# Kernel optimization log

Measured on AMD Instinct MI355X. Metric: run time of the kernel, lower is better.

## Reference

```python
import jax, jax.numpy as jnp
import numpy as np

B = 32768          # batch
LATENT = 128       # latent_dim
H = 100            # hidden_size
VOCAB = 20         # VOCAB_SIZE_EXPRESSION
EXPR_LEN = 21      # EXPR_LENGTH_EXPRESSION


def setup_inputs() -> dict:
    key = jax.random.key(0)
    ks = jax.random.split(key, 17)
    s = 0.1
    inp = {
        "encoder_hidden": jax.random.normal(ks[0], (B, LATENT), jnp.float32),
        "w_proj": s * jax.random.normal(ks[1], (H, LATENT), jnp.float32),
        "b_proj": s * jax.random.normal(ks[2], (H,), jnp.float32),
        "wih0": s * jax.random.normal(ks[3], (3 * H, H), jnp.float32),
        "whh0": s * jax.random.normal(ks[4], (3 * H, H), jnp.float32),
        "bih0": s * jax.random.normal(ks[5], (3 * H,), jnp.float32),
        "bhh0": s * jax.random.normal(ks[6], (3 * H,), jnp.float32),
        "wih1": s * jax.random.normal(ks[7], (3 * H, H), jnp.float32),
        "whh1": s * jax.random.normal(ks[8], (3 * H, H), jnp.float32),
        "bih1": s * jax.random.normal(ks[9], (3 * H,), jnp.float32),
        "bhh1": s * jax.random.normal(ks[10], (3 * H,), jnp.float32),
        "wih2": s * jax.random.normal(ks[11], (3 * H, H), jnp.float32),
        "whh2": s * jax.random.normal(ks[12], (3 * H, H), jnp.float32),
        "bih2": s * jax.random.normal(ks[13], (3 * H,), jnp.float32),
        "bhh2": s * jax.random.normal(ks[14], (3 * H,), jnp.float32),
        "w_out": s * jax.random.normal(ks[15], (VOCAB, H), jnp.float32),
        "b_out": s * jax.random.normal(ks[16], (VOCAB,), jnp.float32),
    }
    return inp


def _gru_cell(gx, h, whh, bhh):
    # gx: precomputed input gates [B, 3H]; h: [B, H]
    gh = h @ whh.T + bhh
    gxr, gxz, gxn = jnp.split(gx, 3, axis=-1)
    ghr, ghz, ghn = jnp.split(gh, 3, axis=-1)
    r = jax.nn.sigmoid(gxr + ghr)
    z = jax.nn.sigmoid(gxz + ghz)
    n = jnp.tanh(gxn + r * ghn)
    return (1.0 - z) * n + z * h


def reference(encoder_hidden, w_proj, b_proj,
              wih0, whh0, bih0, bhh0,
              wih1, whh1, bih1, bhh1,
              wih2, whh2, bih2, bhh2,
              w_out, b_out):
    # decoder_context: same input fed to the GRU at every timestep
    x0 = encoder_hidden @ w_proj.T + b_proj            # [B, H]
    gx0 = x0 @ wih0.T + bih0                           # layer-0 input gates, constant over time

    h_init = jnp.zeros((3, x0.shape[0], H), x0.dtype)  # (num_layers, B, H)

    def step(carry, _):
        h0, h1, h2 = carry
        h0n = _gru_cell(gx0, h0, whh0, bhh0)
        gx1 = h0n @ wih1.T + bih1
        h1n = _gru_cell(gx1, h1, whh1, bhh1)
        gx2 = h1n @ wih2.T + bih2
        h2n = _gru_cell(gx2, h2, whh2, bhh2)
        logits = h2n @ w_out.T + b_out                 # [B, VOCAB]
        return (h0n, h1n, h2n), logits

    _, outs = jax.lax.scan(step, (h_init[0], h_init[1], h_init[2]), None, length=EXPR_LEN)
    return jnp.transpose(outs, (1, 0, 2))              # [B, EXPR_LEN, VOCAB]
```

## Files before the change

kernel.cpp:

```cpp
#include <hip/hip_runtime.h>


#define NTHR 512
#define NBLK 256
#define ROWS_PB 128

#define OFF_PROJ 0
#define OFF_IH0  14336
#define OFF_HH0  57344
#define OFF_IH1  100352
#define OFF_HH1  143360
#define OFF_IH2  186368
#define OFF_HH2  229376
#define OFF_OUT  272384
#define WP_TOTAL 276480

#define X0_OFF   0
#define H0_OFF   16384
#define H1_OFF   32768
#define H2_OFF   49152
#define SMEM_U16 65536

using frag8 = __attribute__((ext_vector_type(8))) short;
using frag4 = __attribute__((ext_vector_type(4))) short;
using f32x4 = __attribute__((ext_vector_type(4))) float;

struct G4 { frag8 a, b, c, d; };

__device__ __forceinline__ unsigned short f2b(float f) {
    union { float f; unsigned u; } v; v.f = f;
    unsigned r = v.u + 0x7FFF + ((v.u >> 16) & 1);
    return (unsigned short)(r >> 16);
}
__device__ __forceinline__ float b2f(unsigned short b) {
    union { unsigned u; float f; } v; v.u = ((unsigned)b) << 16; return v.f;
}

__device__ __forceinline__ f32x4 mfma32(frag8 a, frag8 b, f32x4 c) {
    return __builtin_amdgcn_mfma_f32_16x16x32_bf16(a, b, c, 0, 0, 0);
}
__device__ __forceinline__ f32x4 dot4(const G4& w, const G4& s, f32x4 acc) {
    acc = mfma32(w.a, s.a, acc); acc = mfma32(w.b, s.b, acc);
    acc = mfma32(w.c, s.c, acc); return mfma32(w.d, s.d, acc);
}
__device__ __forceinline__ void pin(G4& w) {
    asm volatile("" : "+v"(w.a), "+v"(w.b), "+v"(w.c), "+v"(w.d));
}

__global__ void prep_kernel(const float* __restrict__ w_proj,
    const float* __restrict__ wih0, const float* __restrict__ bih0,
    const float* __restrict__ whh0, const float* __restrict__ bhh0,
    const float* __restrict__ wih1, const float* __restrict__ bih1,
    const float* __restrict__ whh1, const float* __restrict__ bhh1,
    const float* __restrict__ wih2, const float* __restrict__ bih2,
    const float* __restrict__ whh2, const float* __restrict__ bhh2,
    const float* __restrict__ w_out, const float* __restrict__ b_out,
    unsigned short* __restrict__ dst)
{
    const float LOG2E  = 1.4426950408889634f;
    const float LOG2E2 = 2.8853900817779268f;
    int idx = blockIdx.x * 256 + threadIdx.x;
    if (idx >= WP_TOTAL) return;
    float v = 0.f;
    if (idx < OFF_IH0) {
        int n = idx >> 7, k = idx & 127;
        if (n < 100) v = w_proj[n * 128 + k];
    } else if (idx < OFF_OUT) {
        int r = idx - OFF_IH0;
        int mi = r / 43008;
        int e  = r - mi * 43008;
        int n = e >> 7, k = e & 127;
        int g = n / 112, nn = n - g * 112;
        if (nn < 100) {
            const float* W; const float* Bv;
            switch (mi) {
                case 0: W = wih0; Bv = bih0; break;
                case 1: W = whh0; Bv = bhh0; break;
                case 2: W = wih1; Bv = bih1; break;
                case 3: W = whh1; Bv = bhh1; break;
                case 4: W = wih2; Bv = bih2; break;
                default: W = whh2; Bv = bhh2; break;
            }
            if (k < 100) v = W[(g * 100 + nn) * 100 + k];
            else if (k == 100) v = Bv[g * 100 + nn];
            v *= (g == 2) ? LOG2E2 : LOG2E;
        }
    } else {
        int e = idx - OFF_OUT;
        int n = e >> 7, k = e & 127;
        if (n < 20) {
            if (k < 100) v = w_out[n * 100 + k];
            else if (k == 100) v = b_out[n];
        }
    }
    dst[idx] = f2b(v);
}

__device__ __forceinline__ int hsw(int buf, int grp, int r, int cu) {
    int row = grp * 16 + r;
    return buf + row * 128 + ((((cu >> 3) ^ (row & 7)) << 3) | (cu & 7));
}
__device__ __forceinline__ G4 ldSG4(const unsigned short* sm, int buf, int grp, int c16, int g4) {
    const unsigned short* p = sm + buf + (grp * 16 + c16) * 128;
    int x = c16 & 7;
    G4 s;
    s.a = *(const frag8*)(p + ((g4 ^ x) << 3));
    s.b = *(const frag8*)(p + (((4 + g4) ^ x) << 3));
    s.c = *(const frag8*)(p + (((8 + g4) ^ x) << 3));
    s.d = *(const frag8*)(p + (((12 + g4) ^ x) << 3));
    return s;
}

__device__ __forceinline__ G4 ldWG4(const unsigned short* __restrict__ m, int g, int ro, int g4) {
    const unsigned short* p = m + (size_t)(g * 112 + ro) * 128 + g4 * 8;
    G4 w;
    w.a = *(const frag8*)p;        w.b = *(const frag8*)(p + 32);
    w.c = *(const frag8*)(p + 64); w.d = *(const frag8*)(p + 96);
    return w;
}

__device__ __forceinline__ void logits_one(const unsigned short* sm,
        const G4& O0, const G4& O1, int grp, int lt,
        float* __restrict__ out, int rbase, int c16, int g4) {
    G4 L = ldSG4(sm, H2_OFF, grp, c16, g4);
    f32x4 a0 = {0.f, 0.f, 0.f, 0.f}, a1 = a0;
    a0 = dot4(O0, L, a0);
    a1 = dot4(O1, L, a1);
    float* po = out + (size_t)(rbase + grp * 16 + c16) * 420 + lt * 20;
    *(f32x4*)(po + g4 * 4) = a0;
    if (g4 == 0) *(f32x4*)(po + 16) = a1;
}

template<bool PH0>
__device__ __forceinline__ void gru_phase(unsigned short* sm, int HS, int HD,
    const unsigned short* __restrict__ wih, const unsigned short* __restrict__ whh,
    const G4* O, int lt, float* __restrict__ out, int rbase,
    bool owner, bool vald, int c16, int g4, int ro, int nbase)
{
    __syncthreads();
    frag4 rp[8], zp[8], hn[8];
    if (owner) {
        G4 Wi = ldWG4(wih, 0, ro, g4), Wh = ldWG4(whh, 0, ro, g4);
        pin(Wi); pin(Wh);
#pragma unroll
        for (int grp = 0; grp < 8; ++grp) {
            G4 S = ldSG4(sm, HS, grp, c16, g4);
            G4 D = ldSG4(sm, HD, grp, c16, g4);
            f32x4 a = {0.f, 0.f, 0.f, 0.f};
            a = dot4(Wi, S, a); a = dot4(Wh, D, a);
#pragma unroll
            for (int j = 0; j < 4; ++j)
                rp[grp][j] = (short)f2b(__builtin_amdgcn_rcpf(1.f + __builtin_amdgcn_exp2f(-a[j])));
        }
        Wi = ldWG4(wih, 1, ro, g4); Wh = ldWG4(whh, 1, ro, g4);
        pin(Wi); pin(Wh);
#pragma unroll
        for (int grp = 0; grp < 8; ++grp) {
            G4 S = ldSG4(sm, HS, grp, c16, g4);
            G4 D = ldSG4(sm, HD, grp, c16, g4);
            f32x4 a = {0.f, 0.f, 0.f, 0.f};
            a = dot4(Wi, S, a); a = dot4(Wh, D, a);
#pragma unroll
            for (int j = 0; j < 4; ++j)
                zp[grp][j] = (short)f2b(__builtin_amdgcn_rcpf(1.f + __builtin_amdgcn_exp2f(-a[j])));
        }
        Wi = ldWG4(wih, 2, ro, g4); Wh = ldWG4(whh, 2, ro, g4);
        pin(Wi); pin(Wh);
#pragma unroll
        for (int grp = 0; grp < 8; ++grp) {
            G4 S = ldSG4(sm, HS, grp, c16, g4);
            G4 D = ldSG4(sm, HD, grp, c16, g4);
            f32x4 ax = {0.f, 0.f, 0.f, 0.f}, ah = ax;
            ax = dot4(Wi, S, ax); ah = dot4(Wh, D, ah);
            frag4 hold = *(const frag4*)(sm + hsw(HD, grp, c16, nbase));
#pragma unroll
            for (int j = 0; j < 4; ++j) {
                float r  = b2f((unsigned short)rp[grp][j]);
                float z  = b2f((unsigned short)zp[grp][j]);
                float y  = ax[j] + r * ah[j];
                float nn = 1.f - 2.f * __builtin_amdgcn_rcpf(1.f + __builtin_amdgcn_exp2f(y));
                float ho = b2f((unsigned short)hold[j]);
                hn[grp][j] = (short)f2b(nn + z * (ho - nn));
            }
        }
    } else if (PH0 && lt >= 0) {
#pragma unroll 1
        for (int grp = 0; grp < 8; ++grp)
            logits_one(sm, O[0], O[1], grp, lt, out, rbase, c16, g4);
    }
    __syncthreads();
    if (owner && vald) {
#pragma unroll
        for (int grp = 0; grp < 8; ++grp)
            *(frag4*)(sm + hsw(HD, grp, c16, nbase)) = hn[grp];
    }
}

__global__ void __launch_bounds__(NTHR, 2) rnn_kernel(
    const float* __restrict__ enc,
    const float* __restrict__ b_proj,
    const unsigned short* __restrict__ wp,
    float* __restrict__ out)
{
    __shared__ unsigned short sm[SMEM_U16];
    const int tid  = threadIdx.x;
    const int lane = tid & 63;
    const int wid  = tid >> 6;
    const int c16  = lane & 15;
    const int g4   = lane >> 4;
    const int rbase = blockIdx.x * ROWS_PB;
    const bool owner = (wid < 7);
    const int tw    = owner ? wid : 0;
    const int ro    = tw * 16 + c16;
    const int nbase = tw * 16 + g4 * 4;
    const bool vald = owner && (nbase < 100);

    for (int i = tid; i < SMEM_U16; i += NTHR) {
        int r  = (i >> 7) & 127;
        int cu = i & 127;
        int lcol = ((((cu >> 3) ^ (r & 7)) << 3) | (cu & 7));
        sm[i] = (lcol == 100) ? (unsigned short)0x3F80 : (unsigned short)0;
    }

    G4 O[2];
    if (!owner) {
        O[0] = ldWG4(wp + OFF_OUT, 0, c16, g4);
        O[1] = ldWG4(wp + OFF_OUT, 0, 16 + c16, g4);
        pin(O[0]); pin(O[1]);
    }
    __syncthreads();

    if (owner) {
        G4 P = ldWG4(wp + OFF_PROJ, 0, ro, g4);
        f32x4 bp = {0.f, 0.f, 0.f, 0.f};
        if (vald) bp = *(const f32x4*)(b_proj + nbase);
#pragma unroll 1
        for (int grp = 0; grp < 8; ++grp) {
            const float* ep = enc + (size_t)(rbase + grp * 16 + c16) * 128 + g4 * 8;
            G4 E;
            {
                frag8 e0, e1, e2, e3;
#pragma unroll
                for (int j = 0; j < 8; ++j) {
                    e0[j] = (short)f2b(ep[j]);      e1[j] = (short)f2b(ep[32 + j]);
                    e2[j] = (short)f2b(ep[64 + j]); e3[j] = (short)f2b(ep[96 + j]);
                }
                E.a = e0; E.b = e1; E.c = e2; E.d = e3;
            }
            f32x4 acc = dot4(P, E, bp);
            if (vald) {
                frag4 xv;
#pragma unroll
                for (int j = 0; j < 4; ++j) xv[j] = (short)f2b(acc[j]);
                *(frag4*)(sm + hsw(X0_OFF, grp, c16, nbase)) = xv;
            }
        }
    }

#pragma unroll 1
    for (int t = 0; t < 21; ++t) {
        gru_phase<true >(sm, X0_OFF, H0_OFF, wp + OFF_IH0, wp + OFF_HH0,
                         O, t - 1, out, rbase, owner, vald, c16, g4, ro, nbase);
        gru_phase<false>(sm, H0_OFF, H1_OFF, wp + OFF_IH1, wp + OFF_HH1,
                         O, -1, out, rbase, owner, vald, c16, g4, ro, nbase);
        gru_phase<false>(sm, H1_OFF, H2_OFF, wp + OFF_IH2, wp + OFF_HH2,
                         O, -1, out, rbase, owner, vald, c16, g4, ro, nbase);
    }

    __syncthreads();
    if (!owner) {
#pragma unroll 1
        for (int grp = 0; grp < 8; ++grp)
            logits_one(sm, O[0], O[1], grp, 20, out, rbase, c16, g4);
    }
}

extern "C" void kernel_launch(void* const* d_in, const int* in_sizes, int n_in,
                              void* d_out, int out_size, void* d_ws, size_t ws_size,
                              hipStream_t stream) {
    const float* enc    = (const float*)d_in[0];
    const float* w_proj = (const float*)d_in[1];
    const float* b_proj = (const float*)d_in[2];
    const float* wih0   = (const float*)d_in[3];
    const float* whh0   = (const float*)d_in[4];
    const float* bih0   = (const float*)d_in[5];
    const float* bhh0   = (const float*)d_in[6];
    const float* wih1   = (const float*)d_in[7];
    const float* whh1   = (const float*)d_in[8];
    const float* bih1   = (const float*)d_in[9];
    const float* bhh1   = (const float*)d_in[10];
    const float* wih2   = (const float*)d_in[11];
    const float* whh2   = (const float*)d_in[12];
    const float* bih2   = (const float*)d_in[13];
    const float* bhh2   = (const float*)d_in[14];
    const float* w_out  = (const float*)d_in[15];
    const float* b_out  = (const float*)d_in[16];
    unsigned short* wpd = (unsigned short*)d_ws;
    float* out          = (float*)d_out;

    prep_kernel<<<(WP_TOTAL + 255) / 256, 256, 0, stream>>>(
        w_proj, wih0, bih0, whh0, bhh0, wih1, bih1, whh1, bhh1,
        wih2, bih2, whh2, bhh2, w_out, b_out, wpd);

    rnn_kernel<<<NBLK, NTHR, 0, stream>>>(enc, b_proj, wpd, out);
}
```

Measured before the change: 524.7 us.

## Double block size and split row groups across two wave sets

Raises the block to 1024 threads with 16 waves, so two sets of 8 waves each handle half of the 128 rows (4 row groups instead of 8). Each set has 7 GRU-owner waves and its own logits wave. This halves the per-wave serial work and register arrays per phase, but moves from 2 blocks per CU to 1 block per CU. The aim is shorter critical paths between barriers, at the cost of loading the weights twice per block and syncing more waves at each barrier.

```diff
diff --git a/kernel.cpp b/kernel.cpp
--- a/kernel.cpp
+++ b/kernel.cpp
@@ -1,9 +1,10 @@
 #include <hip/hip_runtime.h>
 
 
-#define NTHR 512
+#define NTHR 1024
 #define NBLK 256
 #define ROWS_PB 128
+#define NGRP 4
 
 #define OFF_PROJ 0
 #define OFF_IH0  14336
@@ -135,39 +136,42 @@
 __device__ __forceinline__ void gru_phase(unsigned short* sm, int HS, int HD,
     const unsigned short* __restrict__ wih, const unsigned short* __restrict__ whh,
     const G4* O, int lt, float* __restrict__ out, int rbase,
-    bool owner, bool vald, int c16, int g4, int ro, int nbase)
+    bool owner, bool vald, bool logw, int gbase, int c16, int g4, int ro, int nbase)
 {
     __syncthreads();
-    frag4 rp[8], zp[8], hn[8];
+    frag4 rp[NGRP], zp[NGRP], hn[NGRP];
     if (owner) {
         G4 Wi = ldWG4(wih, 0, ro, g4), Wh = ldWG4(whh, 0, ro, g4);
         pin(Wi); pin(Wh);
 #pragma unroll
-        for (int grp = 0; grp < 8; ++grp) {
+        for (int q = 0; q < NGRP; ++q) {
+            int grp = gbase + q;
             G4 S = ldSG4(sm, HS, grp, c16, g4);
             G4 D = ldSG4(sm, HD, grp, c16, g4);
             f32x4 a = {0.f, 0.f, 0.f, 0.f};
             a = dot4(Wi, S, a); a = dot4(Wh, D, a);
 #pragma unroll
             for (int j = 0; j < 4; ++j)
-                rp[grp][j] = (short)f2b(__builtin_amdgcn_rcpf(1.f + __builtin_amdgcn_exp2f(-a[j])));
+                rp[q][j] = (short)f2b(__builtin_amdgcn_rcpf(1.f + __builtin_amdgcn_exp2f(-a[j])));
         }
         Wi = ldWG4(wih, 1, ro, g4); Wh = ldWG4(whh, 1, ro, g4);
         pin(Wi); pin(Wh);
 #pragma unroll
-        for (int grp = 0; grp < 8; ++grp) {
+        for (int q = 0; q < NGRP; ++q) {
+            int grp = gbase + q;
             G4 S = ldSG4(sm, HS, grp, c16, g4);
             G4 D = ldSG4(sm, HD, grp, c16, g4);
             f32x4 a = {0.f, 0.f, 0.f, 0.f};
             a = dot4(Wi, S, a); a = dot4(Wh, D, a);
 #pragma unroll
             for (int j = 0; j < 4; ++j)
-                zp[grp][j] = (short)f2b(__builtin_amdgcn_rcpf(1.f + __builtin_amdgcn_exp2f(-a[j])));
+                zp[q][j] = (short)f2b(__builtin_amdgcn_rcpf(1.f + __builtin_amdgcn_exp2f(-a[j])));
         }
         Wi = ldWG4(wih, 2, ro, g4); Wh = ldWG4(whh, 2, ro, g4);
         pin(Wi); pin(Wh);
 #pragma unroll
-        for (int grp = 0; grp < 8; ++grp) {
+        for (int q = 0; q < NGRP; ++q) {
+            int grp = gbase + q;
             G4 S = ldSG4(sm, HS, grp, c16, g4);
             G4 D = ldSG4(sm, HD, grp, c16, g4);
             f32x4 ax = {0.f, 0.f, 0.f, 0.f}, ah = ax;
@@ -175,28 +179,28 @@
             frag4 hold = *(const frag4*)(sm + hsw(HD, grp, c16, nbase));
 #pragma unroll
             for (int j = 0; j < 4; ++j) {
-                float r  = b2f((unsigned short)rp[grp][j]);
-                float z  = b2f((unsigned short)zp[grp][j]);
+                float r  = b2f((unsigned short)rp[q][j]);
+                float z  = b2f((unsigned short)zp[q][j]);
                 float y  = ax[j] + r * ah[j];
                 float nn = 1.f - 2.f * __builtin_amdgcn_rcpf(1.f + __builtin_amdgcn_exp2f(y));
                 float ho = b2f((unsigned short)hold[j]);
-                hn[grp][j] = (short)f2b(nn + z * (ho - nn));
+                hn[q][j] = (short)f2b(nn + z * (ho - nn));
             }
         }
-    } else if (PH0 && lt >= 0) {
+    } else if (PH0 && logw && lt >= 0) {
 #pragma unroll 1
-        for (int grp = 0; grp < 8; ++grp)
-            logits_one(sm, O[0], O[1], grp, lt, out, rbase, c16, g4);
+        for (int q = 0; q < NGRP; ++q)
+            logits_one(sm, O[0], O[1], gbase + q, lt, out, rbase, c16, g4);
     }
     __syncthreads();
     if (owner && vald) {
 #pragma unroll
-        for (int grp = 0; grp < 8; ++grp)
-            *(frag4*)(sm + hsw(HD, grp, c16, nbase)) = hn[grp];
-    }
-}
-
-__global__ void __launch_bounds__(NTHR, 2) rnn_kernel(
+        for (int q = 0; q < NGRP; ++q)
+            *(frag4*)(sm + hsw(HD, gbase + q, c16, nbase)) = hn[q];
+    }
+}
+
+__global__ void __launch_bounds__(NTHR, 1) rnn_kernel(
     const float* __restrict__ enc,
     const float* __restrict__ b_proj,
     const unsigned short* __restrict__ wp,
@@ -209,8 +213,10 @@
     const int c16  = lane & 15;
     const int g4   = lane >> 4;
     const int rbase = blockIdx.x * ROWS_PB;
-    const bool owner = (wid < 7);
-    const int tw    = owner ? wid : 0;
+    const int tw    = wid & 7;
+    const bool owner = (tw < 7);
+    const bool logw  = !owner;
+    const int gbase = (wid >= 8) ? NGRP : 0;
     const int ro    = tw * 16 + c16;
     const int nbase = tw * 16 + g4 * 4;
     const bool vald = owner && (nbase < 100);
@@ -223,7 +229,7 @@
     }
 
     G4 O[2];
-    if (!owner) {
+    if (logw) {
         O[0] = ldWG4(wp + OFF_OUT, 0, c16, g4);
         O[1] = ldWG4(wp + OFF_OUT, 0, 16 + c16, g4);
         pin(O[0]); pin(O[1]);
@@ -235,7 +241,8 @@
         f32x4 bp = {0.f, 0.f, 0.f, 0.f};
         if (vald) bp = *(const f32x4*)(b_proj + nbase);
 #pragma unroll 1
-        for (int grp = 0; grp < 8; ++grp) {
+        for (int q = 0; q < NGRP; ++q) {
+            int grp = gbase + q;
             const float* ep = enc + (size_t)(rbase + grp * 16 + c16) * 128 + g4 * 8;
             G4 E;
             {
@@ -260,18 +267,18 @@
 #pragma unroll 1
     for (int t = 0; t < 21; ++t) {
         gru_phase<true >(sm, X0_OFF, H0_OFF, wp + OFF_IH0, wp + OFF_HH0,
-                         O, t - 1, out, rbase, owner, vald, c16, g4, ro, nbase);
+                         O, t - 1, out, rbase, owner, vald, logw, gbase, c16, g4, ro, nbase);
         gru_phase<false>(sm, H0_OFF, H1_OFF, wp + OFF_IH1, wp + OFF_HH1,
-                         O, -1, out, rbase, owner, vald, c16, g4, ro, nbase);
+                         O, -1, out, rbase, owner, vald, logw, gbase, c16, g4, ro, nbase);
         gru_phase<false>(sm, H1_OFF, H2_OFF, wp + OFF_IH2, wp + OFF_HH2,
-                         O, -1, out, rbase, owner, vald, c16, g4, ro, nbase);
+                         O, -1, out, rbase, owner, vald, logw, gbase, c16, g4, ro, nbase);
     }
 
     __syncthreads();
-    if (!owner) {
+    if (logw) {
 #pragma unroll 1
-        for (int grp = 0; grp < 8; ++grp)
-            logits_one(sm, O[0], O[1], grp, 20, out, rbase, c16, g4);
+        for (int q = 0; q < NGRP; ++q)
+            logits_one(sm, O[0], O[1], gbase + q, 20, out, rbase, c16, g4);
     }
 }
 
```

After: 920.6 us. 75.5% more time.

## Precompute layer-0 input gates in registers and rotate hidden-state buffers

Applied to the files above, without the earlier changes.

Layer-0 input gates (x0·Wih0) are computed once before the time loop and kept in registers as bf16, so each step only does the recurrent matmul for layer 0. Hidden states now use a rotating set of four shared-memory buffers, with writes going to a spare buffer. This removes the second __syncthreads per phase and the register staging of new states. The cost is extra register pressure from holding the gx array (24 frag4 per thread), which could reduce occupancy or cause spills.

```diff
diff --git a/kernel.cpp b/kernel.cpp
--- a/kernel.cpp
+++ b/kernel.cpp
@@ -15,10 +15,6 @@
 #define OFF_OUT  272384
 #define WP_TOTAL 276480
 
-#define X0_OFF   0
-#define H0_OFF   16384
-#define H1_OFF   32768
-#define H2_OFF   49152
 #define SMEM_U16 65536
 
 using frag8 = __attribute__((ext_vector_type(8))) short;
@@ -119,10 +115,10 @@
     return w;
 }
 
-__device__ __forceinline__ void logits_one(const unsigned short* sm,
+__device__ __forceinline__ void logits_one(const unsigned short* sm, int h2buf,
         const G4& O0, const G4& O1, int grp, int lt,
         float* __restrict__ out, int rbase, int c16, int g4) {
-    G4 L = ldSG4(sm, H2_OFF, grp, c16, g4);
+    G4 L = ldSG4(sm, h2buf, grp, c16, g4);
     f32x4 a0 = {0.f, 0.f, 0.f, 0.f}, a1 = a0;
     a0 = dot4(O0, L, a0);
     a1 = dot4(O1, L, a1);
@@ -131,68 +127,68 @@
     if (g4 == 0) *(f32x4*)(po + 16) = a1;
 }
 
-template<bool PH0>
-__device__ __forceinline__ void gru_phase(unsigned short* sm, int HS, int HD,
+template<bool L0, bool PH0>
+__device__ __forceinline__ void gru_phase(unsigned short* sm,
+    int HS, int HD, int HW, int h2buf,
     const unsigned short* __restrict__ wih, const unsigned short* __restrict__ whh,
+    const frag4 (&gx)[3][8],
     const G4* O, int lt, float* __restrict__ out, int rbase,
     bool owner, bool vald, int c16, int g4, int ro, int nbase)
 {
     __syncthreads();
-    frag4 rp[8], zp[8], hn[8];
     if (owner) {
-        G4 Wi = ldWG4(wih, 0, ro, g4), Wh = ldWG4(whh, 0, ro, g4);
-        pin(Wi); pin(Wh);
-#pragma unroll
-        for (int grp = 0; grp < 8; ++grp) {
-            G4 S = ldSG4(sm, HS, grp, c16, g4);
-            G4 D = ldSG4(sm, HD, grp, c16, g4);
-            f32x4 a = {0.f, 0.f, 0.f, 0.f};
-            a = dot4(Wi, S, a); a = dot4(Wh, D, a);
-#pragma unroll
-            for (int j = 0; j < 4; ++j)
-                rp[grp][j] = (short)f2b(__builtin_amdgcn_rcpf(1.f + __builtin_amdgcn_exp2f(-a[j])));
-        }
-        Wi = ldWG4(wih, 1, ro, g4); Wh = ldWG4(whh, 1, ro, g4);
-        pin(Wi); pin(Wh);
-#pragma unroll
-        for (int grp = 0; grp < 8; ++grp) {
-            G4 S = ldSG4(sm, HS, grp, c16, g4);
-            G4 D = ldSG4(sm, HD, grp, c16, g4);
-            f32x4 a = {0.f, 0.f, 0.f, 0.f};
-            a = dot4(Wi, S, a); a = dot4(Wh, D, a);
-#pragma unroll
-            for (int j = 0; j < 4; ++j)
-                zp[grp][j] = (short)f2b(__builtin_amdgcn_rcpf(1.f + __builtin_amdgcn_exp2f(-a[j])));
-        }
-        Wi = ldWG4(wih, 2, ro, g4); Wh = ldWG4(whh, 2, ro, g4);
-        pin(Wi); pin(Wh);
-#pragma unroll
-        for (int grp = 0; grp < 8; ++grp) {
-            G4 S = ldSG4(sm, HS, grp, c16, g4);
-            G4 D = ldSG4(sm, HD, grp, c16, g4);
-            f32x4 ax = {0.f, 0.f, 0.f, 0.f}, ah = ax;
-            ax = dot4(Wi, S, ax); ah = dot4(Wh, D, ah);
-            frag4 hold = *(const frag4*)(sm + hsw(HD, grp, c16, nbase));
-#pragma unroll
-            for (int j = 0; j < 4; ++j) {
-                float r  = b2f((unsigned short)rp[grp][j]);
-                float z  = b2f((unsigned short)zp[grp][j]);
-                float y  = ax[j] + r * ah[j];
-                float nn = 1.f - 2.f * __builtin_amdgcn_rcpf(1.f + __builtin_amdgcn_exp2f(y));
-                float ho = b2f((unsigned short)hold[j]);
-                hn[grp][j] = (short)f2b(nn + z * (ho - nn));
+        frag4 rp[8], zp[8];
+#pragma unroll
+        for (int g = 0; g < 2; ++g) {
+            G4 Wh = ldWG4(whh, g, ro, g4); pin(Wh);
+            G4 Wi;
+            if (!L0) { Wi = ldWG4(wih, g, ro, g4); pin(Wi); }
+#pragma unroll
+            for (int grp = 0; grp < 8; ++grp) {
+                G4 D = ldSG4(sm, HD, grp, c16, g4);
+                f32x4 a = {0.f, 0.f, 0.f, 0.f};
+                a = dot4(Wh, D, a);
+                if (!L0) { G4 S = ldSG4(sm, HS, grp, c16, g4); a = dot4(Wi, S, a); }
+#pragma unroll
+                for (int j = 0; j < 4; ++j) {
+                    float v = a[j];
+                    if (L0) v += b2f((unsigned short)gx[g][grp][j]);
+                    float act = __builtin_amdgcn_rcpf(1.f + __builtin_amdgcn_exp2f(-v));
+                    if (g == 0) rp[grp][j] = (short)f2b(act);
+                    else        zp[grp][j] = (short)f2b(act);
+                }
+            }
+        }
+        {
+            G4 Wh = ldWG4(whh, 2, ro, g4); pin(Wh);
+            G4 Wi;
+            if (!L0) { Wi = ldWG4(wih, 2, ro, g4); pin(Wi); }
+#pragma unroll
+            for (int grp = 0; grp < 8; ++grp) {
+                G4 D = ldSG4(sm, HD, grp, c16, g4);
+                f32x4 ah = {0.f, 0.f, 0.f, 0.f};
+                ah = dot4(Wh, D, ah);
+                f32x4 ax = {0.f, 0.f, 0.f, 0.f};
+                if (!L0) { G4 S = ldSG4(sm, HS, grp, c16, g4); ax = dot4(Wi, S, ax); }
+                frag4 hold = *(const frag4*)(sm + hsw(HD, grp, c16, nbase));
+                frag4 hn;
+#pragma unroll
+                for (int j = 0; j < 4; ++j) {
+                    float r  = b2f((unsigned short)rp[grp][j]);
+                    float z  = b2f((unsigned short)zp[grp][j]);
+                    float xn = L0 ? b2f((unsigned short)gx[2][grp][j]) : ax[j];
+                    float y  = xn + r * ah[j];
+                    float nn = 1.f - 2.f * __builtin_amdgcn_rcpf(1.f + __builtin_amdgcn_exp2f(y));
+                    float ho = b2f((unsigned short)hold[j]);
+                    hn[j] = (short)f2b(nn + z * (ho - nn));
+                }
+                if (vald) *(frag4*)(sm + hsw(HW, grp, c16, nbase)) = hn;
             }
         }
     } else if (PH0 && lt >= 0) {
 #pragma unroll 1
         for (int grp = 0; grp < 8; ++grp)
-            logits_one(sm, O[0], O[1], grp, lt, out, rbase, c16, g4);
-    }
-    __syncthreads();
-    if (owner && vald) {
-#pragma unroll
-        for (int grp = 0; grp < 8; ++grp)
-            *(frag4*)(sm + hsw(HD, grp, c16, nbase)) = hn[grp];
+            logits_one(sm, h2buf, O[0], O[1], grp, lt, out, rbase, c16, g4);
     }
 }
 
@@ -215,6 +211,8 @@
     const int nbase = tw * 16 + g4 * 4;
     const bool vald = owner && (nbase < 100);
 
+    int bh0 = 0, bh1 = 16384, bh2 = 32768, bsp = 49152;
+
     for (int i = tid; i < SMEM_U16; i += NTHR) {
         int r  = (i >> 7) & 127;
         int cu = i & 127;
@@ -252,26 +250,45 @@
                 frag4 xv;
 #pragma unroll
                 for (int j = 0; j < 4; ++j) xv[j] = (short)f2b(acc[j]);
-                *(frag4*)(sm + hsw(X0_OFF, grp, c16, nbase)) = xv;
+                *(frag4*)(sm + hsw(bsp, grp, c16, nbase)) = xv;
+            }
+        }
+    }
+    __syncthreads();
+
+    frag4 gx[3][8];
+    if (owner) {
+#pragma unroll
+        for (int g = 0; g < 3; ++g) {
+            G4 Wi = ldWG4(wp + OFF_IH0, g, ro, g4); pin(Wi);
+#pragma unroll
+            for (int grp = 0; grp < 8; ++grp) {
+                G4 S = ldSG4(sm, bsp, grp, c16, g4);
+                f32x4 a = {0.f, 0.f, 0.f, 0.f};
+                a = dot4(Wi, S, a);
+#pragma unroll
+                for (int j = 0; j < 4; ++j) gx[g][grp][j] = (short)f2b(a[j]);
             }
         }
     }
 
 #pragma unroll 1
     for (int t = 0; t < 21; ++t) {
-        gru_phase<true >(sm, X0_OFF, H0_OFF, wp + OFF_IH0, wp + OFF_HH0,
-                         O, t - 1, out, rbase, owner, vald, c16, g4, ro, nbase);
-        gru_phase<false>(sm, H0_OFF, H1_OFF, wp + OFF_IH1, wp + OFF_HH1,
-                         O, -1, out, rbase, owner, vald, c16, g4, ro, nbase);
-        gru_phase<false>(sm, H1_OFF, H2_OFF, wp + OFF_IH2, wp + OFF_HH2,
-                         O, -1, out, rbase, owner, vald, c16, g4, ro, nbase);
+        gru_phase<true,  true >(sm, 0,   bh0, bsp, bh2, wp + OFF_IH0, wp + OFF_HH0,
+                                gx, O, t - 1, out, rbase, owner, vald, c16, g4, ro, nbase);
+        gru_phase<false, false>(sm, bsp, bh1, bh0, 0,   wp + OFF_IH1, wp + OFF_HH1,
+                                gx, O, -1, out, rbase, owner, vald, c16, g4, ro, nbase);
+        gru_phase<false, false>(sm, bh0, bh2, bh1, 0,   wp + OFF_IH2, wp + OFF_HH2,
+                                gx, O, -1, out, rbase, owner, vald, c16, g4, ro, nbase);
+        int t0 = bh0, t1 = bh1, t2 = bh2;
+        bh0 = bsp; bh1 = t0; bh2 = t1; bsp = t2;
     }
 
     __syncthreads();
     if (!owner) {
 #pragma unroll 1
         for (int grp = 0; grp < 8; ++grp)
-            logits_one(sm, O[0], O[1], grp, 20, out, rbase, c16, g4);
+            logits_one(sm, bh2, O[0], O[1], grp, 20, out, rbase, c16, g4);
     }
 }
 
```

Result: slower. 710.2 us (+35.4%).
